# Kernel tuning notes

Hardware: AMD Instinct MI355X
Metric: run time of the kernel (lower is better)

## Reference

```python
import jax, jax.numpy as jnp
import numpy as np

N = 20000   # nodes
E = 320000  # edges (avg degree 16)
K = 3       # Chebyshev order


def _glorot(key, shape):
    fan_in, fan_out = shape[-2], shape[-1]
    lim = (6.0 / (fan_in + fan_out)) ** 0.5
    return jax.random.uniform(key, shape, minval=-lim, maxval=lim, dtype=jnp.float32)


def setup_inputs() -> dict:
    key = jax.random.key(0)
    ks = jax.random.split(key, 8)
    v = jax.random.normal(ks[0], (N, 86), dtype=jnp.float32)
    edges = jax.random.randint(ks[1], (2, E), 0, N, dtype=jnp.int32)
    W1 = _glorot(ks[2], (K, 86, 128));  b1 = jnp.zeros((128,), jnp.float32)
    W2 = _glorot(ks[3], (K, 128, 256)); b2 = jnp.zeros((256,), jnp.float32)
    W3 = _glorot(ks[4], (K, 256, 512)); b3 = jnp.zeros((512,), jnp.float32)
    return {"v": v, "edges": edges, "W1": W1, "b1": b1,
            "W2": W2, "b2": b2, "W3": W3, "b3": b3}


def _cheb_norm(edges, n):
    # PyG ChebConv with sym norm, lambda_max=2: L_hat = L - I = -D^-1/2 A D^-1/2
    # (diagonal entries from get_laplacian (+1) and add_self_loops (-1) cancel).
    # Self loops are removed before computing the Laplacian -> mask them out.
    row, col = edges[0], edges[1]
    w = (row != col).astype(jnp.float32)
    deg = jax.ops.segment_sum(w, row, num_segments=n)
    dinv = jnp.where(deg > 0, jax.lax.rsqrt(jnp.maximum(deg, 1e-12)), 0.0)
    norm_w = -dinv[row] * w * dinv[col]  # [E]
    return row, col, norm_w


def _cheb_conv(x, row, col, norm_w, W, b):
    # W: [K, in, out]
    def prop(z):  # L_hat @ z via edge gather + segment scatter-add
        return jax.ops.segment_sum(norm_w[:, None] * z[col], row, num_segments=x.shape[0])
    Tx0 = x
    out = Tx0 @ W[0]
    Tx1 = prop(Tx0)
    out = out + Tx1 @ W[1]
    Tx2 = 2.0 * prop(Tx1) - Tx0
    out = out + Tx2 @ W[2]
    return out + b


def reference(v, edges, W1, b1, W2, b2, W3, b3):
    row, col, norm_w = _cheb_norm(edges, v.shape[0])
    nk = jax.random.key(42)
    x1 = jax.nn.relu(_cheb_conv(v, row, col, norm_w, W1, b1))
    x1 = x1 * jax.random.normal(jax.random.fold_in(nk, 1), x1.shape, x1.dtype)
    x2 = jax.nn.relu(_cheb_conv(x1, row, col, norm_w, W2, b2))
    x2 = x2 * jax.random.normal(jax.random.fold_in(nk, 2), x2.shape, x2.dtype)
    x3 = jax.nn.relu(_cheb_conv(x2, row, col, norm_w, W3, b3))
    x3 = x3 * jax.random.normal(jax.random.fold_in(nk, 3), x3.shape, x3.dtype)
    return (x1, x2, x3)
```

## Files before the change

### kernel.cpp

```cpp
#include <hip/hip_runtime.h>
#include <stdint.h>
#include <math.h>

#define DEV static __device__ __forceinline__

typedef __attribute__((ext_vector_type(8))) short bf16x8;
typedef __attribute__((ext_vector_type(4))) float f32x4;
typedef __attribute__((ext_vector_type(8))) unsigned short u16x8;
typedef __attribute__((ext_vector_type(2))) unsigned int u32x2;
typedef __attribute__((ext_vector_type(4))) unsigned int u32x4;

DEV uint32_t rotl32(uint32_t v, int d) { return (v << d) | (v >> (32 - d)); }

DEV void threefry2x32(uint32_t k0, uint32_t k1, uint32_t& x0, uint32_t& x1) {
  const uint32_t k2 = k0 ^ k1 ^ 0x1BD11BDAu;
  x0 += k0; x1 += k1;
#define TFR(R) { x0 += x1; x1 = rotl32(x1, R) ^ x0; }
  TFR(13) TFR(15) TFR(26) TFR(6)
  x0 += k1; x1 += k2 + 1u;
  TFR(17) TFR(29) TFR(16) TFR(24)
  x0 += k2; x1 += k0 + 2u;
  TFR(13) TFR(15) TFR(26) TFR(6)
  x0 += k0; x1 += k1 + 3u;
  TFR(17) TFR(29) TFR(16) TFR(24)
  x0 += k1; x1 += k2 + 4u;
  TFR(13) TFR(15) TFR(26) TFR(6)
  x0 += k2; x1 += k0 + 5u;
#undef TFR
}

DEV float erfinv_f32(float x) {
  float w = -log1pf(-x * x);
  float p;
  if (w < 5.0f) {
    w -= 2.5f;
    p = 2.81022636e-08f;
    p = fmaf(p, w, 3.43273939e-07f);
    p = fmaf(p, w, -3.5233877e-06f);
    p = fmaf(p, w, -4.39150654e-06f);
    p = fmaf(p, w, 0.00021858087f);
    p = fmaf(p, w, -0.00125372503f);
    p = fmaf(p, w, -0.00417768164f);
    p = fmaf(p, w, 0.246640727f);
    p = fmaf(p, w, 1.50140941f);
  } else {
    w = sqrtf(w) - 3.0f;
    p = -0.000200214257f;
    p = fmaf(p, w, 0.000100950558f);
    p = fmaf(p, w, 0.00134934322f);
    p = fmaf(p, w, -0.00367342844f);
    p = fmaf(p, w, 0.00573950773f);
    p = fmaf(p, w, -0.0076224613f);
    p = fmaf(p, w, 0.00943887047f);
    p = fmaf(p, w, 1.00167406f);
    p = fmaf(p, w, 2.83297682f);
  }
  return p * x;
}

DEV float normal_from_bits(uint32_t bits) {
  float f = __uint_as_float((bits >> 9) | 0x3F800000u) - 1.0f;
  const float lo = -0.99999994f;
  float u = fmaf(f, 2.0f, lo);
  u = fmaxf(u, lo);
  return 1.41421356f * erfinv_f32(u);
}

DEV unsigned short f2bf(float f) {
  uint32_t u = __float_as_uint(f);
  uint32_t r = u + 0x7FFFu + ((u >> 16) & 1u);
  return (unsigned short)(r >> 16);
}

DEV float bf2f(uint32_t h) { return __uint_as_float(h << 16); }

DEV float4 noise4(uint32_t f0, uint32_t f1, uint32_t i4) {
  uint32_t base = i4 * 4u;
  float4 r;
  { uint32_t a = 0u, b = base + 0u; threefry2x32(f0, f1, a, b); r.x = normal_from_bits(a ^ b); }
  { uint32_t a = 0u, b = base + 1u; threefry2x32(f0, f1, a, b); r.y = normal_from_bits(a ^ b); }
  { uint32_t a = 0u, b = base + 2u; threefry2x32(f0, f1, a, b); r.z = normal_from_bits(a ^ b); }
  { uint32_t a = 0u, b = base + 3u; threefry2x32(f0, f1, a, b); r.w = normal_from_bits(a ^ b); }
  return r;
}

DEV void noise_fill(unsigned short* __restrict__ nb, int n4_begin, int n4_end, int fold,
                    int gbase, int gstride) {
  uint32_t f0k = 0u, f1k = (uint32_t)fold;
  threefry2x32(0u, 42u, f0k, f1k);
  for (int i4 = n4_begin + gbase; i4 < n4_end; i4 += gstride) {
    float4 r = noise4(f0k, f1k, (uint32_t)i4);
    u32x2 u;
    u.x = (uint32_t)f2bf(r.x) | ((uint32_t)f2bf(r.y) << 16);
    u.y = (uint32_t)f2bf(r.z) | ((uint32_t)f2bf(r.w) << 16);
    *(u32x2*)&nb[(size_t)i4 * 4] = u;
  }
}

__global__ void count_kernel(const int* __restrict__ rows, const int* __restrict__ cols,
                             int* __restrict__ counts, int* __restrict__ degs, int E) {
  int e = blockIdx.x * blockDim.x + threadIdx.x;
  if (e < E) {
    int r = rows[e];
    atomicAdd(&counts[r], 1);
    if (r != cols[e]) atomicAdd(&degs[r], 1);
  }
}

#define SCAN_T 1024
__global__ __launch_bounds__(SCAN_T) void scan_kernel(const int* __restrict__ counts,
                                                      int* __restrict__ row_ptr,
                                                      int* __restrict__ cursor, int N) {
  __shared__ int sa[SCAN_T], sb[SCAN_T];
  const int t = threadIdx.x;
  const int CH = (N + SCAN_T - 1) / SCAN_T;
  int base = t * CH;
  int psum = 0;
  for (int k = 0; k < CH; ++k) {
    int idx = base + k;
    if (idx < N) psum += counts[idx];
  }
  sa[t] = psum;
  __syncthreads();
  int* src = sa; int* dst = sb;
  for (int off = 1; off < SCAN_T; off <<= 1) {
    int v = src[t];
    if (t >= off) v += src[t - off];
    dst[t] = v;
    __syncthreads();
    int* tmp = src; src = dst; dst = tmp;
  }
  int running = src[t] - psum;
  for (int k = 0; k < CH; ++k) {
    int idx = base + k;
    if (idx < N) {
      row_ptr[idx] = running;
      cursor[idx] = running;
      running += counts[idx];
    }
  }
  if (t == SCAN_T - 1) row_ptr[N] = running;
}

__global__ void fill_kernel(const int* __restrict__ rows, const int* __restrict__ cols,
                            const int* __restrict__ degs, int* __restrict__ cursor,
                            float2* __restrict__ ecv, int E) {
  int e = blockIdx.x * blockDim.x + threadIdx.x;
  if (e < E) {
    int r = rows[e], c = cols[e];
    int dr = degs[r], dc = degs[c];
    float w = (r != c && dr > 0 && dc > 0) ? -rsqrtf((float)dr) * rsqrtf((float)dc) : 0.0f;
    int pos = atomicAdd(&cursor[r], 1);
    ecv[pos] = make_float2(__int_as_float(c), w);
  }
}

__global__ void prep_kernel(const float* __restrict__ v,
                            const float* __restrict__ W1, const float* __restrict__ W2,
                            const float* __restrict__ W3,
                            unsigned short* __restrict__ vb, unsigned short* __restrict__ wt1,
                            unsigned short* __restrict__ wt2, unsigned short* __restrict__ wt3,
                            unsigned short* __restrict__ nb1, int n1_total4, int N) {
  noise_fill(nb1, 0, n1_total4, 1, blockIdx.x * 256 + (int)threadIdx.x, gridDim.x * 256);

  int i = blockIdx.x * 256 + threadIdx.x;
  int nv = N * 96;
  if (i < nv) {
    int r = i / 96, k = i % 96;
    vb[i] = (k < 86) ? f2bf(v[(size_t)r * 86 + k]) : (unsigned short)0;
    return;
  }
  i -= nv;
  if (i < 3 * 128 * 96) {
    int k = i % 96, o = (i / 96) % 128, p = i / (96 * 128);
    float val = 0.0f;
    if (k < 86) {
      if (p == 0)      val = W1[((size_t)0 * 86 + k) * 128 + o] - W1[((size_t)2 * 86 + k) * 128 + o];
      else if (p == 1) val = W1[((size_t)1 * 86 + k) * 128 + o];
      else             val = 2.0f * W1[((size_t)2 * 86 + k) * 128 + o];
    }
    wt1[i] = (k < 86) ? f2bf(val) : (unsigned short)0;
    return;
  }
  i -= 3 * 128 * 96;
  if (i < 3 * 256 * 128) {
    int k = i % 128, o = (i / 128) % 256, p = i / (128 * 256);
    float val;
    if (p == 0)      val = W2[((size_t)0 * 128 + k) * 256 + o] - W2[((size_t)2 * 128 + k) * 256 + o];
    else if (p == 1) val = W2[((size_t)1 * 128 + k) * 256 + o];
    else             val = 2.0f * W2[((size_t)2 * 128 + k) * 256 + o];
    wt2[i] = f2bf(val);
    return;
  }
  i -= 3 * 256 * 128;
  if (i < 3 * 512 * 256) {
    int k = i % 256, o = (i / 256) % 512, p = i / (256 * 512);
    float val;
    if (p == 0)      val = W3[((size_t)0 * 256 + k) * 512 + o] - W3[((size_t)2 * 256 + k) * 512 + o];
    else if (p == 1) val = W3[((size_t)1 * 256 + k) * 512 + o];
    else             val = 2.0f * W3[((size_t)2 * 256 + k) * 512 + o];
    wt3[i] = f2bf(val);
  }
}

DEV void ld8(const unsigned short* __restrict__ base, size_t off, float* v) {
  uint4 u = *(const uint4*)(base + off);
  v[0] = bf2f(u.x & 0xffffu); v[1] = bf2f(u.x >> 16);
  v[2] = bf2f(u.y & 0xffffu); v[3] = bf2f(u.y >> 16);
  v[4] = bf2f(u.z & 0xffffu); v[5] = bf2f(u.z >> 16);
  v[6] = bf2f(u.w & 0xffffu); v[7] = bf2f(u.w >> 16);
}

DEV void gather_node(const int* __restrict__ row_ptr, const float2* __restrict__ ecv,
                     const unsigned short* __restrict__ xsrc, int sstride, int fl,
                     int node, float* acc) {
  const int s = row_ptr[node], e = row_ptr[node + 1];
  int j = s;
  for (; j + 8 <= e; j += 8) {
    float2 cw[8];
    float vv[8][8];
#pragma unroll
    for (int q = 0; q < 8; ++q) cw[q] = ecv[j + q];
#pragma unroll
    for (int q = 0; q < 8; ++q)
      ld8(xsrc, (size_t)__float_as_int(cw[q].x) * sstride + fl, vv[q]);
#pragma unroll
    for (int q = 0; q < 8; ++q)
#pragma unroll
      for (int z = 0; z < 8; ++z) acc[z] = fmaf(cw[q].y, vv[q][z], acc[z]);
  }
  for (; j + 2 <= e; j += 2) {
    float2 cw[2];
    float vv[2][8];
#pragma unroll
    for (int q = 0; q < 2; ++q) cw[q] = ecv[j + q];
#pragma unroll
    for (int q = 0; q < 2; ++q)
      ld8(xsrc, (size_t)__float_as_int(cw[q].x) * sstride + fl, vv[q]);
#pragma unroll
    for (int q = 0; q < 2; ++q)
#pragma unroll
      for (int z = 0; z < 8; ++z) acc[z] = fmaf(cw[q].y, vv[q][z], acc[z]);
  }
  for (; j < e; ++j) {
    float2 cw = ecv[j];
    float vv[8];
    ld8(xsrc, (size_t)__float_as_int(cw.x) * sstride + fl, vv);
#pragma unroll
    for (int z = 0; z < 8; ++z) acc[z] = fmaf(cw.y, vv[z], acc[z]);
  }
}

DEV void store8(unsigned short* __restrict__ outb, size_t ob, const float* acc) {
  u32x4 u;
  u.x = (uint32_t)f2bf(acc[0]) | ((uint32_t)f2bf(acc[1]) << 16);
  u.y = (uint32_t)f2bf(acc[2]) | ((uint32_t)f2bf(acc[3]) << 16);
  u.z = (uint32_t)f2bf(acc[4]) | ((uint32_t)f2bf(acc[5]) << 16);
  u.w = (uint32_t)f2bf(acc[6]) | ((uint32_t)f2bf(acc[7]) << 16);
  *(u32x4*)&outb[ob] = u;
}

template <int LPN, int NL, int FOLD>
__global__ __launch_bounds__(256) void gather_prop(
    const int* __restrict__ row_ptr, const float2* __restrict__ ecv,
    const unsigned short* __restrict__ xsrc, int sstride,
    unsigned short* __restrict__ outb, int N, int Fpad,
    unsigned short* __restrict__ nbuf, int n4_begin, int n4_end) {
  const int wave = threadIdx.x >> 6, lane = threadIdx.x & 63;
  const int sub = lane / LPN;
  const int fl = (lane - sub * LPN) * 8;
  const int node = (blockIdx.x * 4 + wave) * NL + sub;
  if (sub < NL && node < N && fl < Fpad) {
    float acc[8] = {};
    gather_node(row_ptr, ecv, xsrc, sstride, fl, node, acc);
    store8(outb, (size_t)node * Fpad + fl, acc);
  }
  noise_fill(nbuf, n4_begin, n4_end, FOLD, blockIdx.x * 256 + (int)threadIdx.x, gridDim.x * 256);
}

template <int BM, int FPAD, int KS, int OB>
__global__ __launch_bounds__(512, 4) void gemm3_db(
    const unsigned short* __restrict__ A0, const unsigned short* __restrict__ A1,
    const unsigned short* __restrict__ A2,
    const unsigned short* __restrict__ Wt, const float* __restrict__ bias,
    const unsigned short* __restrict__ noise,
    int M, int MT, int O, float* __restrict__ out, unsigned short* __restrict__ outb,
    int obstride) {
  constexpr int BN = 128;
  constexpr int NSP = FPAD / KS;
  constexpr int NSTEP = 3 * NSP;
  constexpr int CPR = KS / 8;
  constexpr int LST = KS + 8;
  constexpr int NA = BM * CPR;
  constexpr int NB = BN * CPR;
  constexpr int ACH = (NA + 511) / 512;
  constexpr int BCH = (NB + 511) / 512;
  constexpr int MFR = BM / 32;
  constexpr int KK = KS / 32;

  const int flat = blockIdx.x;
  const int xcd = flat & 7, idx = flat >> 3;
  const int mtile = xcd + 8 * (idx / OB);
  const int obl = idx - (idx / OB) * OB;
  if (mtile >= MT) return;
  const int bm = mtile * BM;
  const int bo = obl * BN;

  __shared__ unsigned short sA[2][BM * LST];
  __shared__ unsigned short sB[2][BN * LST];

  const int tid = threadIdx.x;
  const int lane = tid & 63;
  const int wave = tid >> 6;
  const int wm = wave >> 2, wo = wave & 3;
  const int l15 = lane & 15;
  const int kg = (lane >> 4) * 8;

  f32x4 acc[MFR][2] = {};
  const unsigned short* As[3] = {A0, A1, A2};

  u16x8 ra0[ACH], rb0[BCH], ra1[ACH], rb1[BCH];

  auto issue = [&](int s, u16x8 (&ra)[ACH], u16x8 (&rb)[BCH]) {
    int p = s / NSP, k0 = (s % NSP) * KS;
    const unsigned short* __restrict__ A = As[p];
    const unsigned short* __restrict__ B = Wt + (size_t)p * O * FPAD;
#pragma unroll
    for (int c = 0; c < ACH; ++c) {
      int idx2 = tid + c * 512;
      if (NA % 512 == 0 || idx2 < NA) {
        int row = idx2 / CPR, ch = (idx2 % CPR) * 8;
        int gm = bm + row; if (gm >= M) gm = M - 1;
        ra[c] = *(const u16x8*)(A + (size_t)gm * FPAD + k0 + ch);
      }
    }
#pragma unroll
    for (int c = 0; c < BCH; ++c) {
      int idx2 = tid + c * 512;
      if (NB % 512 == 0 || idx2 < NB) {
        int row = idx2 / CPR, ch = (idx2 % CPR) * 8;
        rb[c] = *(const u16x8*)(B + (size_t)(bo + row) * FPAD + k0 + ch);
      }
    }
  };

  auto lds_write = [&](int buf, u16x8 (&ra)[ACH], u16x8 (&rb)[BCH]) {
#pragma unroll
    for (int c = 0; c < ACH; ++c) {
      int idx2 = tid + c * 512;
      if (NA % 512 == 0 || idx2 < NA) {
        int row = idx2 / CPR, ch = (idx2 % CPR) * 8;
        *(u16x8*)&sA[buf][row * LST + ch] = ra[c];
      }
    }
#pragma unroll
    for (int c = 0; c < BCH; ++c) {
      int idx2 = tid + c * 512;
      if (NB % 512 == 0 || idx2 < NB) {
        int row = idx2 / CPR, ch = (idx2 % CPR) * 8;
        *(u16x8*)&sB[buf][row * LST + ch] = rb[c];
      }
    }
  };

  auto compute = [&](int buf) {
#pragma unroll
    for (int kk = 0; kk < KK; ++kk) {
      bf16x8 af[MFR], bfr[2];
#pragma unroll
      for (int mi = 0; mi < MFR; ++mi)
        af[mi] = *(const bf16x8*)&sA[buf][(wm * (BM / 2) + mi * 16 + l15) * LST + kk * 32 + kg];
#pragma unroll
      for (int ni = 0; ni < 2; ++ni)
        bfr[ni] = *(const bf16x8*)&sB[buf][(wo * 32 + ni * 16 + l15) * LST + kk * 32 + kg];
#pragma unroll
      for (int mi = 0; mi < MFR; ++mi)
#pragma unroll
        for (int ni = 0; ni < 2; ++ni)
          acc[mi][ni] = __builtin_amdgcn_mfma_f32_16x16x32_bf16(af[mi], bfr[ni], acc[mi][ni], 0, 0, 0);
    }
  };

  issue(0, ra0, rb0);
  issue(1, ra1, rb1);
  lds_write(0, ra0, rb0);
  __syncthreads();

#pragma unroll
  for (int s = 0; s < NSTEP; ++s) {
    if ((s & 1) == 0) {
      if (s + 2 < NSTEP) issue(s + 2, ra0, rb0);
      compute(s & 1);
      if (s + 1 < NSTEP) { lds_write((s + 1) & 1, ra1, rb1); __syncthreads(); }
    } else {
      if (s + 2 < NSTEP) issue(s + 2, ra1, rb1);
      compute(s & 1);
      if (s + 1 < NSTEP) { lds_write((s + 1) & 1, ra0, rb0); __syncthreads(); }
    }
  }

  const int r0 = (lane >> 4) * 4;
#pragma unroll
  for (int mi = 0; mi < MFR; ++mi) {
#pragma unroll
    for (int r = 0; r < 4; ++r) {
      int gm = bm + wm * (BM / 2) + mi * 16 + r0 + r;
      if (gm >= M) continue;
#pragma unroll
      for (int ni = 0; ni < 2; ++ni) {
        int go = bo + wo * 32 + ni * 16 + l15;
        float vv = acc[mi][ni][r] + bias[go];
        vv = vv > 0.0f ? vv : 0.0f;
        float res = vv * bf2f((uint32_t)noise[(size_t)gm * O + go]);
        out[(size_t)gm * O + go] = res;
        if (outb) outb[(size_t)gm * obstride + go] = f2bf(res);
      }
    }
  }
}

extern "C" void kernel_launch(void* const* d_in, const int* in_sizes, int n_in,
                              void* d_out, int out_size, void* d_ws, size_t ws_size,
                              hipStream_t stream) {
  const float* v    = (const float*)d_in[0];
  const int*  edges = (const int*)d_in[1];
  const float* W1 = (const float*)d_in[2];
  const float* b1 = (const float*)d_in[3];
  const float* W2 = (const float*)d_in[4];
  const float* b2 = (const float*)d_in[5];
  const float* W3 = (const float*)d_in[6];
  const float* b3 = (const float*)d_in[7];
  float* out = (float*)d_out;

  const int N = in_sizes[0] / 86;
  const int E = in_sizes[1] / 2;
  const int* rows = edges;
  const int* cols = edges + E;

  uintptr_t cur = (uintptr_t)d_ws;
  auto alloc = [&](size_t bytes) {
    cur = (cur + 15) & ~(uintptr_t)15;
    void* p = (void*)cur;
    cur += bytes;
    return p;
  };
  float2* ecv          = (float2*)alloc((size_t)E * 8);
  int* counts          = (int*)alloc((size_t)N * 4);
  int* degs            = (int*)alloc((size_t)N * 4);
  int* row_ptr         = (int*)alloc((size_t)(N + 1) * 4);
  int* cursor          = (int*)alloc((size_t)N * 4);
  unsigned short* tx1b = (unsigned short*)alloc((size_t)N * 256 * 2);
  unsigned short* tx2b = (unsigned short*)alloc((size_t)N * 256 * 2);
  unsigned short* vb   = (unsigned short*)alloc((size_t)N * 96 * 2);
  unsigned short* x1b  = (unsigned short*)alloc((size_t)N * 128 * 2);
  unsigned short* x2b  = (unsigned short*)alloc((size_t)N * 256 * 2);
  unsigned short* wt1  = (unsigned short*)alloc((size_t)3 * 128 * 96 * 2);
  unsigned short* wt2  = (unsigned short*)alloc((size_t)3 * 256 * 128 * 2);
  unsigned short* wt3  = (unsigned short*)alloc((size_t)3 * 512 * 256 * 2);
  unsigned short* nb2  = (unsigned short*)alloc((size_t)N * 256 * 2);
  unsigned short* nb3  = (unsigned short*)alloc((size_t)N * 512 * 2);
  unsigned short* nb1  = nb3;

  float* x1 = out;
  float* x2 = x1 + (size_t)N * 128;
  float* x3 = x2 + (size_t)N * 256;

  hipMemsetAsync(counts, 0, (size_t)2 * N * sizeof(int), stream);
  count_kernel<<<(E + 255) / 256, 256, 0, stream>>>(rows, cols, counts, degs, E);
  scan_kernel<<<1, SCAN_T, 0, stream>>>(counts, row_ptr, cursor, N);
  fill_kernel<<<(E + 255) / 256, 256, 0, stream>>>(rows, cols, degs, cursor, ecv, E);
  {
    int total = N * 96 + 3 * 128 * 96 + 3 * 256 * 128 + 3 * 512 * 256;
    prep_kernel<<<(total + 255) / 256, 256, 0, stream>>>(v, W1, W2, W3, vb, wt1, wt2, wt3,
                                                         nb1, N * 128 / 4, N);
  }

  const int t2 = N * 256 / 4, h2 = t2 / 2;
  const int t3 = N * 512 / 4, q3 = t3 / 4;

  {
    int pb = (N + 15) / 16;
    gather_prop<12, 4, 2><<<pb, 256, 0, stream>>>(row_ptr, ecv, vb, 96, tx1b, N, 96, nb2, 0, h2);
    gather_prop<12, 4, 2><<<pb, 256, 0, stream>>>(row_ptr, ecv, tx1b, 96, tx2b, N, 96, nb2, h2, t2);
    int mt = (N + 63) / 64;
    int grid = 8 * ((mt + 7) / 8) * 1;
    gemm3_db<64, 96, 32, 1><<<grid, 512, 0, stream>>>(vb, tx1b, tx2b, wt1, b1, nb1,
                                                      N, mt, 128, x1, x1b, 128);
  }
  {
    int pb = (N + 15) / 16;
    gather_prop<16, 4, 3><<<pb, 256, 0, stream>>>(row_ptr, ecv, x1b, 128, tx1b, N, 128, nb3, 0, q3);
    gather_prop<16, 4, 3><<<pb, 256, 0, stream>>>(row_ptr, ecv, tx1b, 128, tx2b, N, 128, nb3, q3, 2 * q3);
    int mt = (N + 127) / 128;
    int grid = 8 * ((mt + 7) / 8) * 2;
    gemm3_db<128, 128, 64, 2><<<grid, 512, 0, stream>>>(x1b, tx1b, tx2b, wt2, b2, nb2,
                                                        N, mt, 256, x2, x2b, 256);
  }
  {
    int pb = (N + 7) / 8;
    gather_prop<32, 2, 3><<<pb, 256, 0, stream>>>(row_ptr, ecv, x2b, 256, tx1b, N, 256, nb3, 2 * q3, 3 * q3);
    gather_prop<32, 2, 3><<<pb, 256, 0, stream>>>(row_ptr, ecv, tx1b, 256, tx2b, N, 256, nb3, 3 * q3, t3);
    int mt = (N + 127) / 128;
    int grid = 8 * ((mt + 7) / 8) * 4;
    gemm3_db<128, 256, 64, 4><<<grid, 512, 0, stream>>>(x2b, tx1b, tx2b, wt3, b3, nb3,
                                                        N, mt, 512, x3, nullptr, 0);
  }
}
```

Measured before the change: 356.7 us.

## Slice gather features by XCD and move layer-3 noise generation into prep

Adds a gather kernel that splits the feature dimension into 64-wide slices and maps each slice to a fixed XCD via the block index, so each XCD's L2 caches only its slice of the source features during the random neighbor gathers. The layer-2 and layer-3 propagations use this kernel. Layer-3 noise generation moves out of the gather kernels into the prep kernel, and nb1 gets its own buffer instead of aliasing nb3. The gathers become pure memory kernels, but prep now does much more threefry work serially up front, and extra memory is allocated.

```diff
diff --git a/kernel.cpp b/kernel.cpp
--- a/kernel.cpp
+++ b/kernel.cpp
@@ -160,10 +160,14 @@
                             const float* __restrict__ W3,
                             unsigned short* __restrict__ vb, unsigned short* __restrict__ wt1,
                             unsigned short* __restrict__ wt2, unsigned short* __restrict__ wt3,
-                            unsigned short* __restrict__ nb1, int n1_total4, int N) {
-  noise_fill(nb1, 0, n1_total4, 1, blockIdx.x * 256 + (int)threadIdx.x, gridDim.x * 256);
-
-  int i = blockIdx.x * 256 + threadIdx.x;
+                            unsigned short* __restrict__ nb1, int n1_total4,
+                            unsigned short* __restrict__ nb3, int n3_total4, int N) {
+  int g = blockIdx.x * 256 + threadIdx.x;
+  int gs = gridDim.x * 256;
+  noise_fill(nb1, 0, n1_total4, 1, g, gs);
+  noise_fill(nb3, 0, n3_total4, 3, g, gs);
+
+  int i = g;
   int nv = N * 96;
   if (i < nv) {
     int r = i / 96, k = i % 96;
@@ -276,6 +280,26 @@
     store8(outb, (size_t)node * Fpad + fl, acc);
   }
   noise_fill(nbuf, n4_begin, n4_end, FOLD, blockIdx.x * 256 + (int)threadIdx.x, gridDim.x * 256);
+}
+
+template <int G>
+__global__ __launch_bounds__(256) void gather_prop_sl(
+    const int* __restrict__ row_ptr, const float2* __restrict__ ecv,
+    const unsigned short* __restrict__ xsrc, int sstride,
+    unsigned short* __restrict__ outb, int N, int Fpad, int NBK) {
+  const int flat = blockIdx.x;
+  const int xcd = flat & 7, j = flat >> 3;
+  const int slice = xcd / G;
+  const int nb = j * G + (xcd % G);
+  if (nb >= NBK) return;
+  const int wave = threadIdx.x >> 6, lane = threadIdx.x & 63;
+  const int sub = lane >> 3;
+  const int fl = slice * 64 + (lane & 7) * 8;
+  const int node = nb * 32 + wave * 8 + sub;
+  if (node >= N) return;
+  float acc[8] = {};
+  gather_node(row_ptr, ecv, xsrc, sstride, fl, node, acc);
+  store8(outb, (size_t)node * Fpad + fl, acc);
 }
 
 template <int BM, int FPAD, int KS, int OB>
@@ -457,9 +481,9 @@
   unsigned short* wt1  = (unsigned short*)alloc((size_t)3 * 128 * 96 * 2);
   unsigned short* wt2  = (unsigned short*)alloc((size_t)3 * 256 * 128 * 2);
   unsigned short* wt3  = (unsigned short*)alloc((size_t)3 * 512 * 256 * 2);
+  unsigned short* nb1  = (unsigned short*)alloc((size_t)N * 128 * 2);
   unsigned short* nb2  = (unsigned short*)alloc((size_t)N * 256 * 2);
   unsigned short* nb3  = (unsigned short*)alloc((size_t)N * 512 * 2);
-  unsigned short* nb1  = nb3;
 
   float* x1 = out;
   float* x2 = x1 + (size_t)N * 128;
@@ -472,11 +496,12 @@
   {
     int total = N * 96 + 3 * 128 * 96 + 3 * 256 * 128 + 3 * 512 * 256;
     prep_kernel<<<(total + 255) / 256, 256, 0, stream>>>(v, W1, W2, W3, vb, wt1, wt2, wt3,
-                                                         nb1, N * 128 / 4, N);
-  }
-
+                                                         nb1, N * 128 / 4,
+                                                         nb3, N * 512 / 4, N);
+  }
+
+  const int NBK = (N + 31) / 32;
   const int t2 = N * 256 / 4, h2 = t2 / 2;
-  const int t3 = N * 512 / 4, q3 = t3 / 4;
 
   {
     int pb = (N + 15) / 16;
@@ -488,18 +513,18 @@
                                                       N, mt, 128, x1, x1b, 128);
   }
   {
-    int pb = (N + 15) / 16;
-    gather_prop<16, 4, 3><<<pb, 256, 0, stream>>>(row_ptr, ecv, x1b, 128, tx1b, N, 128, nb3, 0, q3);
-    gather_prop<16, 4, 3><<<pb, 256, 0, stream>>>(row_ptr, ecv, tx1b, 128, tx2b, N, 128, nb3, q3, 2 * q3);
+    int pgrid = 8 * ((NBK + 3) / 4);
+    gather_prop_sl<4><<<pgrid, 256, 0, stream>>>(row_ptr, ecv, x1b, 128, tx1b, N, 128, NBK);
+    gather_prop_sl<4><<<pgrid, 256, 0, stream>>>(row_ptr, ecv, tx1b, 128, tx2b, N, 128, NBK);
     int mt = (N + 127) / 128;
     int grid = 8 * ((mt + 7) / 8) * 2;
     gemm3_db<128, 128, 64, 2><<<grid, 512, 0, stream>>>(x1b, tx1b, tx2b, wt2, b2, nb2,
                                                         N, mt, 256, x2, x2b, 256);
   }
   {
-    int pb = (N + 7) / 8;
-    gather_prop<32, 2, 3><<<pb, 256, 0, stream>>>(row_ptr, ecv, x2b, 256, tx1b, N, 256, nb3, 2 * q3, 3 * q3);
-    gather_prop<32, 2, 3><<<pb, 256, 0, stream>>>(row_ptr, ecv, tx1b, 256, tx2b, N, 256, nb3, 3 * q3, t3);
+    int pgrid = 8 * ((NBK + 1) / 2);
+    gather_prop_sl<2><<<pgrid, 256, 0, stream>>>(row_ptr, ecv, x2b, 256, tx1b, N, 256, NBK);
+    gather_prop_sl<2><<<pgrid, 256, 0, stream>>>(row_ptr, ecv, tx1b, 256, tx2b, N, 256, NBK);
     int mt = (N + 127) / 128;
     int grid = 8 * ((mt + 7) / 8) * 4;
     gemm3_db<128, 256, 64, 4><<<grid, 512, 0, stream>>>(x2b, tx1b, tx2b, wt3, b3, nb3,
```

Result: slower. 371.0 us (+4.0%).
